# Performance work log

Measured on AMD Instinct MI355X. Metric: run time of the kernel, lower is better.

Reference implementation:

```python
import jax, jax.numpy as jnp
import numpy as np

B, L, DM = 2, 2048, 2048
EXP = 2; DI = EXP * DM          # d_inner = 4096
N = 64                           # d_state
K = 4                            # d_conv
P = 64                           # headdim
H = DI // P                      # n_heads = 64
G = 1                            # n_groups
CONV = DI + 2 * G * N            # 4224
PROJ = 2 * DI + 2 * G * N + H    # 8384
EPS = 1e-6


def setup_inputs() -> dict:
    ks = jax.random.split(jax.random.key(0), 6)
    s = 0.02
    return {
        'u': jax.random.normal(ks[0], (B, L, DM), jnp.float32),
        'ln_w': jnp.ones((DM,), jnp.float32),
        'in_proj_w': jax.random.normal(ks[1], (PROJ, DM), jnp.float32) * s,
        'conv_w': jax.random.normal(ks[2], (K, CONV), jnp.float32) * 0.1,
        'conv_b': jnp.zeros((CONV,), jnp.float32),
        'dt_bias': jax.random.uniform(ks[3], (H,), jnp.float32, 0.0, 1.0),
        'A_log': jnp.log(jnp.arange(1, H + 1, dtype=jnp.float32)),
        'D': jnp.ones((H,), jnp.float32),
        'norm_w': jnp.ones((DI,), jnp.float32),
        'out_proj_w': jax.random.normal(ks[4], (DM, DI), jnp.float32) * s,
    }


def _rmsnorm(x, w, eps=EPS):
    xf = x.astype(jnp.float32)
    v = jnp.mean(xf * xf, axis=-1, keepdims=True)
    return w * (xf * jax.lax.rsqrt(v + eps)).astype(x.dtype)


def reference(u, ln_w, in_proj_w, conv_w, conv_b, dt_bias, A_log, D, norm_w, out_proj_w):
    residual = u
    hs = _rmsnorm(u, ln_w)                                 # input RMSNorm
    zxbcdt = hs @ in_proj_w.T                              # (B,L,PROJ)
    z, xBC, dt = jnp.split(zxbcdt, [DI, DI + CONV], axis=-1)
    # causal depthwise conv1d over time + SiLU
    xp = jnp.pad(xBC, ((0, 0), (K - 1, 0), (0, 0)))
    xc = conv_b + sum(xp[:, k:k + L, :] * conv_w[k] for k in range(K))
    xc = jax.nn.silu(xc)
    x, Bm, Cm = jnp.split(xc, [DI, DI + G * N], axis=-1)
    x = x.reshape(B, L, H, P)
    Bm = jnp.repeat(Bm.reshape(B, L, G, N), H // G, axis=2)  # (B,L,H,N)
    Cm = jnp.repeat(Cm.reshape(B, L, G, N), H // G, axis=2)
    dt = jax.nn.softplus(dt + dt_bias)                       # (B,L,H)
    dA = jnp.exp(dt * (-jnp.exp(A_log)))                     # (B,L,H)
    dtx = dt[..., None] * x                                  # (B,L,H,P)

    def step(h, inp):
        dA_t, dtx_t, B_t, C_t = inp
        # h: (B,H,P,N); h_t = exp(dt*A) h_{t-1} + (dt*x_t) outer B_t
        h = dA_t[:, :, None, None] * h + dtx_t[..., None] * B_t[:, :, None, :]
        y = jnp.einsum('bhpn,bhn->bhp', h, C_t)
        return h, y

    h0 = jnp.zeros((B, H, P, N), jnp.float32)
    _, ys = jax.lax.scan(step, h0, (dA.transpose(1, 0, 2),
                                    dtx.transpose(1, 0, 2, 3),
                                    Bm.transpose(1, 0, 2, 3),
                                    Cm.transpose(1, 0, 2, 3)))
    y = ys.transpose(1, 0, 2, 3) + D[None, None, :, None] * x   # (B,L,H,P)
    # gated RMSNorm: (y * silu(z)) -> rmsnorm
    y = _rmsnorm(y.reshape(B, L, DI) * jax.nn.silu(z), norm_w)
    out = y @ out_proj_w.T
    return residual + out
```

## Files before the change

kernel.cpp:

```cpp
#include <hip/hip_runtime.h>
#include <hip/hip_bf16.h>

typedef __bf16 bf16;
typedef __bf16 bf16x8 __attribute__((ext_vector_type(8)));
typedef float f32x4 __attribute__((ext_vector_type(4)));

#define B_    2
#define L_    2048
#define DM_   2048
#define DI_   4096
#define NST   64
#define PD    64
#define NH    64
#define CONV_ 4224
#define XBCD_ 4288
#define PROJ_ 8384
#define BL_   (B_ * L_)
#define NCHUNK 32
#define EPS_  1e-6f

#define WAITV(n) asm volatile("s_waitcnt vmcnt(" #n ")" ::: "memory")
#define BAR()    __builtin_amdgcn_s_barrier()

__device__ __forceinline__ float block_reduce_sum_256(float v) {
  #pragma unroll
  for (int m = 32; m; m >>= 1) v += __shfl_xor(v, m, 64);
  __shared__ float sred[4];
  int w = threadIdx.x >> 6;
  if ((threadIdx.x & 63) == 0) sred[w] = v;
  __syncthreads();
  return sred[0] + sred[1] + sred[2] + sred[3];
}

__device__ __forceinline__ float silu_f(float x) {
  return x / (1.0f + expf(-x));
}

__device__ __forceinline__ void async16(const bf16* g, bf16* l) {
  __builtin_amdgcn_global_load_lds(
      (__attribute__((address_space(1))) void*)g,
      (__attribute__((address_space(3))) void*)l, 16, 0, 0);
}

__global__ __launch_bounds__(256) void rmsnorm_in_kernel(
    const float* __restrict__ u, const float* __restrict__ w, bf16* __restrict__ hs) {
  int row = blockIdx.x;
  const float* x = u + (size_t)row * DM_;
  int base = threadIdx.x * 8;
  f32x4 v0 = *(const f32x4*)(x + base);
  f32x4 v1 = *(const f32x4*)(x + base + 4);
  float xv[8], ss = 0.f;
  #pragma unroll
  for (int i = 0; i < 4; i++) { xv[i] = v0[i]; xv[4 + i] = v1[i]; }
  #pragma unroll
  for (int i = 0; i < 8; i++) ss += xv[i] * xv[i];
  ss = block_reduce_sum_256(ss);
  float r = rsqrtf(ss / (float)DM_ + EPS_);
  f32x4 w0 = *(const f32x4*)(w + base);
  f32x4 w1 = *(const f32x4*)(w + base + 4);
  bf16x8 o;
  #pragma unroll
  for (int i = 0; i < 4; i++) { o[i] = (bf16)(w0[i] * xv[i] * r); o[4 + i] = (bf16)(w1[i] * xv[4 + i] * r); }
  *(bf16x8*)(hs + (size_t)row * DM_ + base) = o;
}

__global__ __launch_bounds__(256) void convert_w_kernel(
    const float* __restrict__ src, bf16* __restrict__ dst,
    long n_src, long n_dst) {
  long e = ((long)blockIdx.x * 256 + threadIdx.x) * 8;
  if (e >= n_dst) return;
  bf16x8 o;
  if (e < n_src) {
    f32x4 a = *(const f32x4*)(src + e);
    f32x4 b = *(const f32x4*)(src + e + 4);
    #pragma unroll
    for (int q = 0; q < 4; q++) { o[q] = (bf16)a[q]; o[4 + q] = (bf16)b[q]; }
  } else {
    #pragma unroll
    for (int q = 0; q < 8; q++) o[q] = (bf16)0.f;
  }
  *(bf16x8*)(dst + e) = o;
}

template <bool OUT_F32>
__global__ __launch_bounds__(256, 4) void gemm_nt_sb(
    const bf16* __restrict__ A, int lda,
    const bf16* __restrict__ W, int ldw,
    void* __restrict__ Cout, int ldc, const float* __restrict__ resid,
    int N, int K) {
  __shared__ __align__(16) bf16 As[128 * 64];
  __shared__ __align__(16) bf16 Bs[128 * 64];
  int nwg = gridDim.x * gridDim.y;
  int bid = blockIdx.y * gridDim.x + blockIdx.x;
  int q8 = nwg >> 3, r8 = nwg & 7;
  int xcd = bid & 7, loc = bid >> 3;
  int nb = (xcd < r8 ? xcd * (q8 + 1) : r8 * (q8 + 1) + (xcd - r8) * q8) + loc;
  int bn = nb % gridDim.x, bm = nb / gridDim.x;
  int m0 = bm * 128, n0 = bn * 128;
  int tid = threadIdx.x, wave = tid >> 6, lane = tid & 63;
  int wm = (wave >> 1) * 64, wn = (wave & 1) * 64;
  int lm = lane & 15, lk = (lane >> 4) * 8;
  int lr = lane >> 3;
  int cse = ((lane & 7) ^ lr) * 8;
  f32x4 acc[4][4] = {};

  int NT = K / 64;
  for (int t = 0; t < NT; ++t) {
    #pragma unroll
    for (int i = 0; i < 4; ++i) {
      int row = (wave * 4 + i) * 8;
      async16(A + (size_t)(m0 + row + lr) * lda + t * 64 + cse, &As[row * 64]);
      async16(W + (size_t)(n0 + row + lr) * ldw + t * 64 + cse, &Bs[row * 64]);
    }
    WAITV(0);
    BAR();
    #pragma unroll
    for (int ks = 0; ks < 64; ks += 32) {
      bf16x8 af[4], bf[4];
      #pragma unroll
      for (int i = 0; i < 4; ++i) {
        int row = wm + i * 16 + lm;
        af[i] = *(const bf16x8*)&As[row * 64 + ((((ks + lk) >> 3) ^ (row & 7)) << 3)];
      }
      #pragma unroll
      for (int j = 0; j < 4; ++j) {
        int row = wn + j * 16 + lm;
        bf[j] = *(const bf16x8*)&Bs[row * 64 + ((((ks + lk) >> 3) ^ (row & 7)) << 3)];
      }
      #pragma unroll
      for (int i = 0; i < 4; ++i)
        #pragma unroll
        for (int j = 0; j < 4; ++j)
          acc[i][j] = __builtin_amdgcn_mfma_f32_16x16x32_bf16(af[i], bf[j], acc[i][j], 0, 0, 0);
    }
    BAR();
  }
  int r0 = m0 + wm + (lane >> 4) * 4;
  #pragma unroll
  for (int i = 0; i < 4; ++i) {
    #pragma unroll
    for (int j = 0; j < 4; ++j) {
      int col = n0 + wn + j * 16 + lm;
      if (col < N) {
        #pragma unroll
        for (int r = 0; r < 4; ++r) {
          int row = r0 + i * 16 + r;
          size_t idx = (size_t)row * ldc + col;
          float v = acc[i][j][r];
          if (resid) v += resid[idx];
          if (OUT_F32) ((float*)Cout)[idx] = v;
          else         ((bf16*)Cout)[idx]  = (bf16)v;
        }
      }
    }
  }
}

__global__ __launch_bounds__(256) void conv_bc_kernel(
    const bf16* __restrict__ xbcdt, const float* __restrict__ cw,
    const float* __restrict__ cb, bf16* __restrict__ xc) {
  int idx = blockIdx.x * 256 + threadIdx.x;
  if (idx >= BL_ * 16) return;
  int c8 = idx & 15, t = idx >> 4;
  int l = t % L_;
  int c = DI_ + c8 * 8;
  float acc[8];
  f32x4 bv0 = *(const f32x4*)(cb + c);
  f32x4 bv1 = *(const f32x4*)(cb + c + 4);
  #pragma unroll
  for (int q = 0; q < 4; q++) { acc[q] = bv0[q]; acc[4 + q] = bv1[q]; }
  #pragma unroll
  for (int k = 0; k < 4; k++) {
    int ls = l + k - 3;
    if (ls >= 0) {
      const bf16* xp = xbcdt + (size_t)(t + k - 3) * XBCD_ + c;
      bf16x8 xv = *(const bf16x8*)xp;
      f32x4 wv0 = *(const f32x4*)(cw + k * CONV_ + c);
      f32x4 wv1 = *(const f32x4*)(cw + k * CONV_ + c + 4);
      #pragma unroll
      for (int q = 0; q < 4; q++) { acc[q] += (float)xv[q] * wv0[q]; acc[4 + q] += (float)xv[4 + q] * wv1[q]; }
    }
  }
  bf16x8 o;
  #pragma unroll
  for (int q = 0; q < 8; q++) o[q] = (bf16)silu_f(acc[q]);
  *(bf16x8*)(xc + (size_t)t * CONV_ + c) = o;
}

__global__ __launch_bounds__(256) void dt_kernel(
    const bf16* __restrict__ xbcdt, const float* __restrict__ dt_bias,
    float* __restrict__ dtH) {
  int idx = blockIdx.x * 256 + threadIdx.x;
  if (idx >= BL_ * NH) return;
  int h = idx & 63, t = idx >> 6;
  float raw = (float)xbcdt[(size_t)t * XBCD_ + CONV_ + h] + dt_bias[h];
  float v = (raw > 20.f) ? raw : log1pf(expf(raw));
  dtH[(size_t)h * BL_ + t] = v;
}

__global__ __launch_bounds__(256) void atot_kernel(
    const float* __restrict__ dtH, const float* __restrict__ A_log,
    float* __restrict__ Atot) {
  int idx = blockIdx.x * 256 + threadIdx.x;
  if (idx >= B_ * NH * NCHUNK) return;
  int c = idx & 31, rem = idx >> 5;
  int h = rem & 63, b = rem >> 6;
  const float* p = dtH + (size_t)h * BL_ + b * L_ + c * 64;
  float s = 0.f;
  #pragma unroll 8
  for (int i = 0; i < 64; i++) s += p[i];
  Atot[idx] = expf(-expf(A_log[h]) * s);
}

__global__ __launch_bounds__(256) void scan_chunk_mfma(
    bf16* __restrict__ xc, const bf16* __restrict__ xbcdt,
    const float* __restrict__ cw, const float* __restrict__ cb,
    const float* __restrict__ dtH,
    const float* __restrict__ A_log, const float* __restrict__ Dp,
    bf16* __restrict__ Sc) {
  __shared__ bf16 Bs[64][72];
  __shared__ bf16 Cs[64][72];
  __shared__ bf16 Xt[64][72];
  __shared__ bf16 Gh[64][72];
  __shared__ bf16 Gl[64][72];
  __shared__ float dts[64];
  __shared__ float cum[64];
  __shared__ float wsA[64];
  int bi = blockIdx.x;
  int h = bi & 63, c = (bi >> 6) & 31, b = bi >> 11;
  int tid = threadIdx.x;
  int wave = tid >> 6, lane = tid & 63;
  int lm = lane & 15, lk = (lane >> 4) * 8;
  int cl = lane & 15, rw4 = (lane >> 4) * 4;
  int wt = (wave >> 1) * 32, wq = (wave & 1) * 32;
  size_t rowbase = (size_t)b * L_ + c * 64;
  float aA = expf(A_log[h]);
  #pragma unroll
  for (int i = 0; i < 2; i++) {
    int cc = tid + i * 256;
    int s = cc >> 3, e8 = (cc & 7) * 8;
    const bf16* base = xc + (rowbase + s) * CONV_;
    bf16x8 bv = *(const bf16x8*)(base + DI_ + e8);
    bf16x8 cv = *(const bf16x8*)(base + DI_ + NST + e8);
    *(bf16x8*)&Bs[s][e8 ^ (s & 56)] = bv;
    *(bf16x8*)&Cs[s][e8] = cv;
    int col = h * PD + e8;
    int l = c * 64 + s;
    float acc[8];
    f32x4 cb0 = *(const f32x4*)(cb + col);
    f32x4 cb1 = *(const f32x4*)(cb + col + 4);
    #pragma unroll
    for (int q = 0; q < 4; q++) { acc[q] = cb0[q]; acc[4 + q] = cb1[q]; }
    #pragma unroll
    for (int k = 0; k < 4; k++) {
      int ls = l + k - 3;
      if (ls >= 0) {
        const bf16* xp = xbcdt + (rowbase + s + k - 3) * XBCD_ + col;
        bf16x8 xv = *(const bf16x8*)xp;
        f32x4 wv0 = *(const f32x4*)(cw + k * CONV_ + col);
        f32x4 wv1 = *(const f32x4*)(cw + k * CONV_ + col + 4);
        #pragma unroll
        for (int q = 0; q < 4; q++) { acc[q] += (float)xv[q] * wv0[q]; acc[4 + q] += (float)xv[4 + q] * wv1[q]; }
      }
    }
    #pragma unroll
    for (int q = 0; q < 8; q++) Xt[e8 + q][s ^ e8] = (bf16)silu_f(acc[q]);
  }
  if (tid < 64) dts[tid] = dtH[(size_t)h * BL_ + rowbase + tid];
  __syncthreads();
  if (tid < 64) {
    float v = dts[tid];
    #pragma unroll
    for (int off = 1; off < 64; off <<= 1) {
      float o = __shfl_up(v, off, 64);
      if (tid >= off) v += o;
    }
    cum[tid] = v;
  }
  __syncthreads();
  if (tid < 64) wsA[tid] = expf(-aA * (cum[63] - cum[tid])) * dts[tid];
  f32x4 gacc[2][2] = {};
  #pragma unroll
  for (int ks = 0; ks < 64; ks += 32) {
    bf16x8 af[2], bfr[2];
    #pragma unroll
    for (int i = 0; i < 2; i++) af[i] = *(bf16x8*)&Cs[wt + i * 16 + lm][ks + lk];
    #pragma unroll
    for (int j = 0; j < 2; j++) {
      int S = wq + j * 16 + lm;
      bfr[j] = *(bf16x8*)&Bs[S][(ks + lk) ^ (S & 56)];
    }
    #pragma unroll
    for (int i = 0; i < 2; i++)
      #pragma unroll
      for (int j = 0; j < 2; j++)
        gacc[i][j] = __builtin_amdgcn_mfma_f32_16x16x32_bf16(af[i], bfr[j], gacc[i][j], 0, 0, 0);
  }
  #pragma unroll
  for (int i = 0; i < 2; i++) {
    #pragma unroll
    for (int j = 0; j < 2; j++) {
      #pragma unroll
      for (int r = 0; r < 4; r++) {
        int t = wt + i * 16 + rw4 + r;
        int s = wq + j * 16 + cl;
        float g = 0.f;
        if (s <= t) g = gacc[i][j][r] * expf(-aA * (cum[t] - cum[s])) * dts[s];
        bf16 ghi = (bf16)g;
        Gh[t][s] = ghi;
        Gl[t][s] = (bf16)(g - (float)ghi);
      }
    }
  }
  __syncthreads();
  f32x4 yacc[2][2] = {};
  #pragma unroll
  for (int ks = 0; ks < 64; ks += 32) {
    bf16x8 ah[2], al[2], bx[2];
    #pragma unroll
    for (int i = 0; i < 2; i++) {
      ah[i] = *(bf16x8*)&Gh[wt + i * 16 + lm][ks + lk];
      al[i] = *(bf16x8*)&Gl[wt + i * 16 + lm][ks + lk];
    }
    #pragma unroll
    for (int j = 0; j < 2; j++) {
      int P = wq + j * 16 + lm;
      bx[j] = *(bf16x8*)&Xt[P][(ks + lk) ^ (P & 56)];
    }
    #pragma unroll
    for (int i = 0; i < 2; i++)
      #pragma unroll
      for (int j = 0; j < 2; j++) {
        yacc[i][j] = __builtin_amdgcn_mfma_f32_16x16x32_bf16(ah[i], bx[j], yacc[i][j], 0, 0, 0);
        yacc[i][j] = __builtin_amdgcn_mfma_f32_16x16x32_bf16(al[i], bx[j], yacc[i][j], 0, 0, 0);
      }
  }
  float Dv = Dp[h];
  #pragma unroll
  for (int i = 0; i < 2; i++) {
    #pragma unroll
    for (int j = 0; j < 2; j++) {
      int p = wq + j * 16 + cl;
      #pragma unroll
      for (int r = 0; r < 4; r++) {
        int t = wt + i * 16 + rw4 + r;
        float yv = yacc[i][j][r] + Dv * (float)Xt[p][t ^ (p & 56)];
        xc[(rowbase + t) * CONV_ + h * PD + p] = (bf16)yv;
      }
    }
  }
  __syncthreads();
  #pragma unroll
  for (int i = 0; i < 2; i++) {
    int cc = tid + i * 256;
    int n = cc >> 3, s8 = (cc & 7) * 8;
    bf16x8 vh, vl;
    #pragma unroll
    for (int q = 0; q < 8; q++) {
      int s = s8 + q;
      float wb = (float)Bs[s][n ^ (s & 56)] * wsA[s];
      vh[q] = (bf16)wb;
      vl[q] = (bf16)(wb - (float)vh[q]);
    }
    *(bf16x8*)&Gh[n][s8] = vh;
    *(bf16x8*)&Gl[n][s8] = vl;
  }
  __syncthreads();
  f32x4 sacc[2][2] = {};
  #pragma unroll
  for (int ks = 0; ks < 64; ks += 32) {
    bf16x8 ax[2], bh[2], bl[2];
    #pragma unroll
    for (int i = 0; i < 2; i++) {
      int P = wt + i * 16 + lm;
      ax[i] = *(bf16x8*)&Xt[P][(ks + lk) ^ (P & 56)];
    }
    #pragma unroll
    for (int j = 0; j < 2; j++) {
      bh[j] = *(bf16x8*)&Gh[wq + j * 16 + lm][ks + lk];
      bl[j] = *(bf16x8*)&Gl[wq + j * 16 + lm][ks + lk];
    }
    #pragma unroll
    for (int i = 0; i < 2; i++)
      #pragma unroll
      for (int j = 0; j < 2; j++) {
        sacc[i][j] = __builtin_amdgcn_mfma_f32_16x16x32_bf16(ax[i], bh[j], sacc[i][j], 0, 0, 0);
        sacc[i][j] = __builtin_amdgcn_mfma_f32_16x16x32_bf16(ax[i], bl[j], sacc[i][j], 0, 0, 0);
      }
  }
  bf16* scp = Sc + ((((size_t)b * NCHUNK + c) * NH + h) << 12);
  #pragma unroll
  for (int i = 0; i < 2; i++) {
    #pragma unroll
    for (int j = 0; j < 2; j++) {
      int n = wq + j * 16 + cl;
      #pragma unroll
      for (int r = 0; r < 4; r++) {
        int p = wt + i * 16 + rw4 + r;
        scp[p * 64 + n] = (bf16)sacc[i][j][r];
      }
    }
  }
}

__global__ __launch_bounds__(256) void state_scan_kernel(
    bf16* __restrict__ Sc, const float* __restrict__ Atot) {
  __shared__ float At[NCHUNK];
  int bid = blockIdx.x;
  int seg = bid & 15, rem = bid >> 4;
  int e = seg * 256 + threadIdx.x;
  if (threadIdx.x < NCHUNK) At[threadIdx.x] = Atot[(rem << 5) + threadIdx.x];
  __syncthreads();
  int h = rem & 63, b = rem >> 6;
  bf16* p = Sc + ((((size_t)b * NCHUNK) * NH + h) << 12) + e;
  const size_t cstride = (size_t)NH << 12;
  float H = 0.f;
  #pragma unroll 4
  for (int c = 0; c < NCHUNK; ++c) {
    float s = (float)*p;
    *p = (bf16)H;
    H = At[c] * H + s;
    p += cstride;
  }
}

__global__ __launch_bounds__(256) void y_inter_mfma(
    bf16* __restrict__ xc, const float* __restrict__ dtH,
    const float* __restrict__ A_log, const bf16* __restrict__ Sc) {
  __shared__ bf16 Cs[64][72];
  __shared__ bf16 Hs[64][72];
  __shared__ float dts[64];
  __shared__ float eA[64];
  int bi = blockIdx.x;
  int h = bi & 63, c = (bi >> 6) & 31, b = bi >> 11;
  int tid = threadIdx.x;
  int wave = tid >> 6, lane = tid & 63;
  int lm = lane & 15, lk = (lane >> 4) * 8;
  int cl = lane & 15, rw4 = (lane >> 4) * 4;
  int wt = (wave >> 1) * 32, wp = (wave & 1) * 32;
  size_t rowbase = (size_t)b * L_ + c * 64;
  float aA = expf(A_log[h]);
  const bf16* scp = Sc + ((((size_t)b * NCHUNK + c) * NH + h) << 12);
  #pragma unroll
  for (int i = 0; i < 2; i++) {
    int cc = tid + i * 256;
    int s = cc >> 3, e8 = (cc & 7) * 8;
    bf16x8 cv = *(const bf16x8*)(xc + (rowbase + s) * CONV_ + DI_ + NST + e8);
    *(bf16x8*)&Cs[s][e8] = cv;
  }
  {
    int p = tid >> 2, n16 = (tid & 3) * 16;
    *(bf16x8*)&Hs[p][n16]     = *(const bf16x8*)(scp + p * 64 + n16);
    *(bf16x8*)&Hs[p][n16 + 8] = *(const bf16x8*)(scp + p * 64 + n16 + 8);
  }
  if (tid < 64) dts[tid] = dtH[(size_t)h * BL_ + rowbase + tid];
  __syncthreads();
  if (tid < 64) {
    float v = dts[tid];
    #pragma unroll
    for (int off = 1; off < 64; off <<= 1) {
      float o = __shfl_up(v, off, 64);
      if (tid >= off) v += o;
    }
    eA[tid] = expf(-aA * v);
  }
  __syncthreads();
  f32x4 acc[2][2] = {};
  #pragma unroll
  for (int ks = 0; ks < 64; ks += 32) {
    bf16x8 af[2], bfr[2];
    #pragma unroll
    for (int i = 0; i < 2; i++) af[i]  = *(bf16x8*)&Cs[wt + i * 16 + lm][ks + lk];
    #pragma unroll
    for (int j = 0; j < 2; j++) bfr[j] = *(bf16x8*)&Hs[wp + j * 16 + lm][ks + lk];
    #pragma unroll
    for (int i = 0; i < 2; i++)
      #pragma unroll
      for (int j = 0; j < 2; j++)
        acc[i][j] = __builtin_amdgcn_mfma_f32_16x16x32_bf16(af[i], bfr[j], acc[i][j], 0, 0, 0);
  }
  #pragma unroll
  for (int i = 0; i < 2; i++) {
    #pragma unroll
    for (int j = 0; j < 2; j++) {
      int p = wp + j * 16 + cl;
      #pragma unroll
      for (int r = 0; r < 4; r++) {
        int t = wt + i * 16 + rw4 + r;
        size_t gi = (rowbase + t) * CONV_ + h * PD + p;
        xc[gi] = (bf16)((float)xc[gi] + eA[t] * acc[i][j][r]);
      }
    }
  }
}

__global__ __launch_bounds__(256) void gated_norm_kernel(
    const bf16* __restrict__ xc, bf16* __restrict__ zbuf,
    const float* __restrict__ nw) {
  int t = blockIdx.x;
  int base = threadIdx.x * 16;
  const bf16* yr = xc + (size_t)t * CONV_;
  bf16* zr = zbuf + (size_t)t * DI_;
  float tv[16], ss = 0.f;
  #pragma unroll
  for (int i8 = 0; i8 < 2; i8++) {
    bf16x8 yv = *(const bf16x8*)(yr + base + i8 * 8);
    bf16x8 zv = *(const bf16x8*)(zr + base + i8 * 8);
    #pragma unroll
    for (int q = 0; q < 8; q++) {
      float tt = (float)yv[q] * silu_f((float)zv[q]);
      tv[i8 * 8 + q] = tt;
      ss += tt * tt;
    }
  }
  ss = block_reduce_sum_256(ss);
  float r = rsqrtf(ss / (float)DI_ + EPS_);
  #pragma unroll
  for (int i8 = 0; i8 < 2; i8++) {
    f32x4 w0 = *(const f32x4*)(nw + base + i8 * 8);
    f32x4 w1 = *(const f32x4*)(nw + base + i8 * 8 + 4);
    bf16x8 o;
    #pragma unroll
    for (int q = 0; q < 4; q++) {
      o[q]     = (bf16)(w0[q] * tv[i8 * 8 + q] * r);
      o[4 + q] = (bf16)(w1[q] * tv[i8 * 8 + 4 + q] * r);
    }
    *(bf16x8*)(zr + base + i8 * 8) = o;
  }
}

__global__ void ws_report_kernel(float* out, float ws_mb) {
  if (blockIdx.x == 0 && threadIdx.x == 0) out[0] = ws_mb;
}

extern "C" void kernel_launch(void* const* d_in, const int* in_sizes, int n_in,
                              void* d_out, int out_size, void* d_ws, size_t ws_size,
                              hipStream_t stream) {
  const float* u        = (const float*)d_in[0];
  const float* ln_w     = (const float*)d_in[1];
  const float* in_proj  = (const float*)d_in[2];
  const float* conv_w   = (const float*)d_in[3];
  const float* conv_b   = (const float*)d_in[4];
  const float* dt_bias  = (const float*)d_in[5];
  const float* A_log    = (const float*)d_in[6];
  const float* Dp       = (const float*)d_in[7];
  const float* norm_w   = (const float*)d_in[8];
  const float* out_proj = (const float*)d_in[9];
  float* out = (float*)d_out;

  bf16* hs = (bf16*)d_out;

  char* ws = (char*)d_ws;
  size_t off = 0;
  auto alloc = [&](size_t bytes) { char* p = ws + off; off = (off + bytes + 255) & ~(size_t)255; return p; };
  float* dtH  = (float*)alloc((size_t)BL_ * NH * 4);
  float* Atot = (float*)alloc((size_t)B_ * NH * NCHUNK * 4);
  bf16*  wbuf = (bf16*)alloc((size_t)4352 * DM_ * 2);
  bf16*  shbuf= (bf16*)alloc((size_t)BL_ * XBCD_ * 2);
  bf16*  xc   = (bf16*)alloc((size_t)BL_ * CONV_ * 2);
  bf16*  Sc   = (bf16*)alloc((size_t)B_ * NCHUNK * NH * 64 * 64 * 2);
  size_t need = off;

  if (ws_size < need) {
    ws_report_kernel<<<1, 64, 0, stream>>>(out, (float)(ws_size >> 20));
    return;
  }

  bf16* xbcdt = shbuf;
  bf16* zbuf  = shbuf;

  rmsnorm_in_kernel<<<BL_, 256, 0, stream>>>(u, ln_w, hs);

  {
    long nsrc = (long)XBCD_ * DM_, ndst = (long)4352 * DM_;
    convert_w_kernel<<<(int)(ndst / 8 / 256), 256, 0, stream>>>(
        in_proj + (size_t)DI_ * DM_, wbuf, nsrc, ndst);
    gemm_nt_sb<false><<<dim3(4352 / 128, BL_ / 128), 256, 0, stream>>>(
        hs, DM_, wbuf, DM_, xbcdt, XBCD_, nullptr, XBCD_, DM_);
  }
  conv_bc_kernel<<<(BL_ * 16 + 255) / 256, 256, 0, stream>>>(
      xbcdt, conv_w, conv_b, xc);
  dt_kernel<<<(BL_ * NH + 255) / 256, 256, 0, stream>>>(
      xbcdt, dt_bias, dtH);
  atot_kernel<<<(B_ * NH * NCHUNK + 255) / 256, 256, 0, stream>>>(
      dtH, A_log, Atot);
  scan_chunk_mfma<<<B_ * NH * NCHUNK, 256, 0, stream>>>(
      xc, xbcdt, conv_w, conv_b, dtH, A_log, Dp, Sc);
  state_scan_kernel<<<B_ * NH * 16, 256, 0, stream>>>(Sc, Atot);
  y_inter_mfma<<<B_ * NH * NCHUNK, 256, 0, stream>>>(xc, dtH, A_log, Sc);

  {
    long n = (long)DI_ * DM_;
    convert_w_kernel<<<(int)(n / 8 / 256), 256, 0, stream>>>(in_proj, wbuf, n, n);
    gemm_nt_sb<false><<<dim3(DI_ / 128, BL_ / 128), 256, 0, stream>>>(
        hs, DM_, wbuf, DM_, zbuf, DI_, nullptr, DI_, DM_);
  }
  gated_norm_kernel<<<BL_, 256, 0, stream>>>(xc, zbuf, norm_w);

  {
    long n = (long)DM_ * DI_;
    convert_w_kernel<<<(int)(n / 8 / 256), 256, 0, stream>>>(out_proj, wbuf, n, n);
    gemm_nt_sb<true><<<dim3(DM_ / 128, BL_ / 128), 256, 0, stream>>>(
        zbuf, DI_, wbuf, DI_, out, DM_, u, DM_, DI_);
  }
}
```

Before: 544.7 us.

## Double-buffer GEMM shared-memory tiles with K-step 32 to overlap loads

Replaces the single-buffered 64-wide K tile GEMM with a double-buffered 32-wide K tile pipeline. The next tile is prefetched asynchronously while MFMAs consume the current one, and the XOR swizzle is adapted to the narrower rows. This hides global-load latency behind compute, but doubles the number of barriers per K and halves the MFMA work per iteration.

```diff
diff --git a/kernel.cpp b/kernel.cpp
--- a/kernel.cpp
+++ b/kernel.cpp
@@ -83,13 +83,13 @@
 }
 
 template <bool OUT_F32>
-__global__ __launch_bounds__(256, 4) void gemm_nt_sb(
+__global__ __launch_bounds__(256, 4) void gemm_nt_p32(
     const bf16* __restrict__ A, int lda,
     const bf16* __restrict__ W, int ldw,
     void* __restrict__ Cout, int ldc, const float* __restrict__ resid,
     int N, int K) {
-  __shared__ __align__(16) bf16 As[128 * 64];
-  __shared__ __align__(16) bf16 Bs[128 * 64];
+  __shared__ __align__(16) bf16 As[2][128 * 32];
+  __shared__ __align__(16) bf16 Bs[2][128 * 32];
   int nwg = gridDim.x * gridDim.y;
   int bid = blockIdx.y * gridDim.x + blockIdx.x;
   int q8 = nwg >> 3, r8 = nwg & 7;
@@ -99,40 +99,44 @@
   int m0 = bm * 128, n0 = bn * 128;
   int tid = threadIdx.x, wave = tid >> 6, lane = tid & 63;
   int wm = (wave >> 1) * 64, wn = (wave & 1) * 64;
-  int lm = lane & 15, lk = (lane >> 4) * 8;
-  int lr = lane >> 3;
-  int cse = ((lane & 7) ^ lr) * 8;
+  int lm = lane & 15, sl = lane >> 4;
+  int lrs = lane >> 2;
+  int cse = ((lane & 3) ^ ((lane >> 3) & 3)) * 8;
   f32x4 acc[4][4] = {};
 
-  int NT = K / 64;
+  auto stage = [&](int d, int t) {
+    #pragma unroll
+    for (int i = 0; i < 2; ++i) {
+      int ch = wave * 2 + i;
+      int row = ch * 16 + lrs;
+      async16(A + (size_t)(m0 + row) * lda + t * 32 + cse, &As[d][ch * 512]);
+      async16(W + (size_t)(n0 + row) * ldw + t * 32 + cse, &Bs[d][ch * 512]);
+    }
+  };
+
+  int NT = K / 32;
+  stage(0, 0);
   for (int t = 0; t < NT; ++t) {
+    int d = t & 1;
+    if (t + 1 < NT) { stage(d ^ 1, t + 1); WAITV(4); }
+    else            { WAITV(0); }
+    BAR();
+    bf16x8 af[4], bf[4];
     #pragma unroll
     for (int i = 0; i < 4; ++i) {
-      int row = (wave * 4 + i) * 8;
-      async16(A + (size_t)(m0 + row + lr) * lda + t * 64 + cse, &As[row * 64]);
-      async16(W + (size_t)(n0 + row + lr) * ldw + t * 64 + cse, &Bs[row * 64]);
-    }
-    WAITV(0);
-    BAR();
-    #pragma unroll
-    for (int ks = 0; ks < 64; ks += 32) {
-      bf16x8 af[4], bf[4];
-      #pragma unroll
-      for (int i = 0; i < 4; ++i) {
-        int row = wm + i * 16 + lm;
-        af[i] = *(const bf16x8*)&As[row * 64 + ((((ks + lk) >> 3) ^ (row & 7)) << 3)];
-      }
-      #pragma unroll
-      for (int j = 0; j < 4; ++j) {
-        int row = wn + j * 16 + lm;
-        bf[j] = *(const bf16x8*)&Bs[row * 64 + ((((ks + lk) >> 3) ^ (row & 7)) << 3)];
-      }
-      #pragma unroll
-      for (int i = 0; i < 4; ++i)
-        #pragma unroll
-        for (int j = 0; j < 4; ++j)
-          acc[i][j] = __builtin_amdgcn_mfma_f32_16x16x32_bf16(af[i], bf[j], acc[i][j], 0, 0, 0);
-    }
+      int row = wm + i * 16 + lm;
+      af[i] = *(const bf16x8*)&As[d][row * 32 + ((sl ^ ((row >> 1) & 3)) * 8)];
+    }
+    #pragma unroll
+    for (int j = 0; j < 4; ++j) {
+      int row = wn + j * 16 + lm;
+      bf[j] = *(const bf16x8*)&Bs[d][row * 32 + ((sl ^ ((row >> 1) & 3)) * 8)];
+    }
+    #pragma unroll
+    for (int i = 0; i < 4; ++i)
+      #pragma unroll
+      for (int j = 0; j < 4; ++j)
+        acc[i][j] = __builtin_amdgcn_mfma_f32_16x16x32_bf16(af[i], bf[j], acc[i][j], 0, 0, 0);
     BAR();
   }
   int r0 = m0 + wm + (lane >> 4) * 4;
@@ -575,7 +579,7 @@
     long nsrc = (long)XBCD_ * DM_, ndst = (long)4352 * DM_;
     convert_w_kernel<<<(int)(ndst / 8 / 256), 256, 0, stream>>>(
         in_proj + (size_t)DI_ * DM_, wbuf, nsrc, ndst);
-    gemm_nt_sb<false><<<dim3(4352 / 128, BL_ / 128), 256, 0, stream>>>(
+    gemm_nt_p32<false><<<dim3(4352 / 128, BL_ / 128), 256, 0, stream>>>(
         hs, DM_, wbuf, DM_, xbcdt, XBCD_, nullptr, XBCD_, DM_);
   }
   conv_bc_kernel<<<(BL_ * 16 + 255) / 256, 256, 0, stream>>>(
@@ -592,7 +596,7 @@
   {
     long n = (long)DI_ * DM_;
     convert_w_kernel<<<(int)(n / 8 / 256), 256, 0, stream>>>(in_proj, wbuf, n, n);
-    gemm_nt_sb<false><<<dim3(DI_ / 128, BL_ / 128), 256, 0, stream>>>(
+    gemm_nt_p32<false><<<dim3(DI_ / 128, BL_ / 128), 256, 0, stream>>>(
         hs, DM_, wbuf, DM_, zbuf, DI_, nullptr, DI_, DM_);
   }
   gated_norm_kernel<<<BL_, 256, 0, stream>>>(xc, zbuf, norm_w);
@@ -600,7 +604,7 @@
   {
     long n = (long)DM_ * DI_;
     convert_w_kernel<<<(int)(n / 8 / 256), 256, 0, stream>>>(out_proj, wbuf, n, n);
-    gemm_nt_sb<true><<<dim3(DM_ / 128, BL_ / 128), 256, 0, stream>>>(
+    gemm_nt_p32<true><<<dim3(DM_ / 128, BL_ / 128), 256, 0, stream>>>(
         zbuf, DI_, wbuf, DI_, out, DM_, u, DM_, DI_);
   }
 }
```

Result: slower. 596.0 us (+9.4%).
